# Optimization experiments

Measured on AMD Instinct MI355X. Metric: run time of the kernel, lower is better.

Reference implementation:

```python
import jax, jax.numpy as jnp
import numpy as np
from functools import partial

WARMUP = 365   # init kwarg warmup_length
HYDRODT = 1.0  # daily step

# (name, lower, upper) -- stands in for MODEL_PARAM_DICT['sac']['param_range']
PARAM_RANGES = [
    ("KC", 0.1, 1.2), ("PCTIM", 0.0, 0.1), ("ADIMP", 0.0, 0.3),
    ("UZTWM", 10.0, 100.0), ("UZFWM", 10.0, 100.0), ("LZTWM", 50.0, 400.0),
    ("LZFSM", 10.0, 100.0), ("LZFPM", 50.0, 1000.0), ("RSERV", 0.0, 0.3),
    ("PFREE", 0.0, 0.5), ("RIVA", 0.0, 0.1), ("ZPERC", 5.0, 350.0),
    ("REXP", 1.0, 4.0), ("UZK", 0.1, 0.5), ("LZSK", 0.01, 0.35),
    ("LZPK", 0.001, 0.05), ("CI", 0.5, 0.9), ("CGS", 0.95, 0.998),
    ("CGP", 0.98, 0.998), ("KE", 0.0, 1.0), ("XE", 0.0, 0.5),
]
_LO = np.array([r[1] for r in PARAM_RANGES], dtype=np.float32)
_HI = np.array([r[2] for r in PARAM_RANGES], dtype=np.float32)


def _scale_params(parameters):
    ps = _LO + parameters * (_HI - _LO)  # (n_basin, 21)
    return {name: ps[:, i] for i, (name, _, _) in enumerate(PARAM_RANGES)}


def _sac_step(prm, carry, pe_t):
    (auztw, alztw, uztw, uzfw, lztw, lzfs, lzfp, qs, qi, qgs, qgp, mq) = carry
    kc, pctim, adimp = prm["KC"], prm["PCTIM"], prm["ADIMP"]
    uztwm, uzfwm, lztwm = prm["UZTWM"], prm["UZFWM"], prm["LZTWM"]
    lzfsm, lzfpm = prm["LZFSM"], prm["LZFPM"]
    pfree, riva = prm["PFREE"], prm["RIVA"]
    zperc, rexp, uzk = prm["ZPERC"], prm["REXP"], prm["UZK"]
    lzsk, lzpk = prm["LZSK"], prm["LZPK"]
    ci, cgs, cgp, ke, xe = prm["CI"], prm["CGS"], prm["CGP"], prm["KE"], prm["XE"]

    p = jnp.maximum(pe_t[:, 0], 0.0)
    e = jnp.maximum(jnp.nan_to_num(pe_t[:, 1], nan=0.0, posinf=0.0, neginf=0.0), 0.0)
    ep = kc * e
    # --- impervious / alterable-impervious area ---
    roimp = pctim * p
    ae2 = pctim * ep
    ae1 = jnp.minimum(auztw, ep * (auztw / uztwm))
    ae3 = jnp.maximum((ep - ae1) * (alztw / (uztwm + lztwm)), 0.0)
    pav = jnp.maximum(p - (uztwm - (auztw - ae1)), 0.0)
    adsur = jnp.maximum(pav * ((alztw - ae3) / lztwm), 0.0)
    ars = jnp.maximum(pav - adsur + (alztw - ae3) - lztwm, 0.0)
    auztw = jnp.maximum(jnp.minimum(uztwm, auztw - ae1 + p), 0.0)
    alztw = jnp.maximum(jnp.minimum(lztwm, pav - adsur + (alztw - ae3)), 0.0)
    # --- permeable-area evaporation ---
    e1 = jnp.minimum(uztw, ep * (uztw / uztwm))
    e2 = jnp.maximum(jnp.minimum(uzfw, ep - e1), 0.0)
    e3 = jnp.maximum((ep - e1 - e2) * (lztw / (uztwm + lztwm)), 0.0)
    lt1 = jnp.maximum(lztw - e3, 0.0)
    e4 = riva * ep
    et = ae2 + ae1 + ae3 + e1 + e2 + e3 + e4
    adsur_adimp = adsur * adimp
    ars_adimp = ars * adimp
    parea = 1.0 - pctim - adimp
    # --- permeable-area runoff ---
    rs = jnp.maximum(p + (uztw + uzfw - e1 - e2) - (uztwm + uzfwm), 0.0) * parea
    ut = jnp.maximum(jnp.minimum(uztwm, uztw - e1 + p), 0.0)
    uf = jnp.maximum(jnp.minimum(uzfwm, p + (uztw + uzfw - e1 - e2) - ut), 0.0)
    ri = uf * uzk
    uf = jnp.maximum(uf - ri, 0.0)
    # --- percolation into the lower zone ---
    pbase = lzfsm * lzsk + lzfpm * lzpk
    defr = jnp.maximum(1.0 - (lzfs + lzfp + lt1) / (lzfsm + lzfpm + lztwm), 0.0)
    perc = pbase * (1.0 + zperc * jnp.power(defr, rexp)) * uf / uzfwm
    rate = jnp.maximum(jnp.minimum(perc, (lzfsm + lzfpm + lztwm) - (lzfs + lzfp + lt1)), 0.0)
    uf = jnp.maximum(uf - rate, 0.0)
    fx = jnp.maximum(jnp.minimum(lzfsm + lzfpm - (lzfs + lzfp),
                                 jnp.maximum(rate - (lztwm - lt1), rate * pfree)), 0.0)
    perct = rate - fx
    coef = (lzfpm / (lzfsm + lzfpm)) * (2.0 * (1.0 - lzfp / lzfpm)
           / ((1.0 - lzfp / lzfpm) + (1.0 - lzfs / lzfsm)))
    coef = jnp.minimum(coef, 1.0)
    percp = jnp.maximum(jnp.minimum(lzfpm - lzfp,
                                    jnp.maximum(fx - (lzfsm - lzfs), coef * fx)), 0.0)
    percs = jnp.maximum(fx - percp, 0.0)
    lt = jnp.minimum(lt1 + perct, lztwm)
    ls = lzfs + percs
    lp = lzfp + percp
    rgs = ls * lzsk
    ls = jnp.maximum(ls - rgs, 0.0)
    rgp = lp * lzpk
    lp = jnp.maximum(lp - rgp, 0.0)
    # --- area-weighted runoff components ---
    ri_p, rgs_p, rgp_p = ri * parea, rgs * parea, rgp * parea
    rs_tot = roimp + adsur_adimp + ars_adimp + rs
    # --- slope routing: linear reservoirs ---
    i1 = qs + qi + qgs + qgp  # previous-step total channel inflow
    qs_n = rs_tot
    qi_n = ci * qi + (1.0 - ci) * ri_p
    qgs_n = cgs * qgs + (1.0 - cgs) * rgs_p
    qgp_n = cgp * qgp + (1.0 - cgp) * rgp_p
    i2 = qs_n + qi_n + qgs_n + qgp_n
    # --- river routing: Muskingum, single reach (rivernumber = 1) ---
    dt = 0.5 * HYDRODT
    denom = ke * (1.0 - xe) + dt
    c1 = (ke * xe + dt) / denom
    c2 = (dt - ke * xe) / denom
    c3 = (ke * (1.0 - xe) - dt) / denom
    o1 = mq[:, 0]
    o2 = c1 * i1 + c2 * i2 + c3 * o1
    mq_n = o2[:, None]
    carry_n = (auztw, alztw, ut, uf, lt, ls, lp, qs_n, qi_n, qgs_n, qgp_n, mq_n)
    return carry_n, (et, o2)


def _sac_run(p_and_e, parameters, step_wrap=lambda f: f):
    prm = _scale_params(parameters)
    n_basin = parameters.shape[0]
    s01 = jnp.full((n_basin,), 0.01, dtype=p_and_e.dtype)
    carry = tuple(s01 for _ in range(11)) + (jnp.full((n_basin, 1), 0.01, dtype=p_and_e.dtype),)
    step = step_wrap(partial(_sac_step, prm))
    if WARMUP > 0:
        carry, _ = jax.lax.scan(step, carry, p_and_e[:WARMUP])
        carry = jax.tree_util.tree_map(jax.lax.stop_gradient, carry)  # torch no_grad warmup
    _, (e_sim, q_sim) = jax.lax.scan(step, carry, p_and_e[WARMUP:])
    return jnp.stack([q_sim, e_sim])  # (2, n_step, n_basin)


def setup_inputs() -> dict:
    key = jax.random.key(0)
    k1, k2, k3 = jax.random.split(key, 3)
    T, B = 1825, 10000
    prcp = jax.random.uniform(k1, (T, B), minval=0.0, maxval=20.0)  # mm/day
    pet = jax.random.uniform(k3, (T, B), minval=0.0, maxval=6.0)    # mm/day
    p_and_e = jnp.stack([prcp, pet], axis=-1).astype(jnp.float32)
    parameters = jax.random.uniform(k2, (B, 21), minval=0.01, maxval=0.99).astype(jnp.float32)
    return {"p_and_e": p_and_e, "parameters": parameters}


def reference(p_and_e, parameters):
    return _sac_run(p_and_e, parameters)
```

## Files before the change

kernel.cpp:

```cpp
#include <hip/hip_runtime.h>
#include <math.h>

#define T_TOTAL 1825
#define WARMUP_T 365
#define T_OUT (T_TOTAL - WARMUP_T)
#define NB 10000

__global__ __launch_bounds__(64, 1)
void sac_kernel(const float* __restrict__ p_and_e,
                const float* __restrict__ params,
                float* __restrict__ out)
{
    const int b = blockIdx.x * blockDim.x + threadIdx.x;
    if (b >= NB) return;

    const float* pr = params + b * 21;
    const float kc    = 0.1f   + pr[0]  * (1.2f - 0.1f);
    const float pctim = 0.0f   + pr[1]  * (0.1f - 0.0f);
    const float adimp = 0.0f   + pr[2]  * (0.3f - 0.0f);
    const float uztwm = 10.0f  + pr[3]  * (100.0f - 10.0f);
    const float uzfwm = 10.0f  + pr[4]  * (100.0f - 10.0f);
    const float lztwm = 50.0f  + pr[5]  * (400.0f - 50.0f);
    const float lzfsm = 10.0f  + pr[6]  * (100.0f - 10.0f);
    const float lzfpm = 50.0f  + pr[7]  * (1000.0f - 50.0f);
    const float pfree = 0.0f   + pr[9]  * (0.5f - 0.0f);
    const float riva  = 0.0f   + pr[10] * (0.1f - 0.0f);
    const float zperc = 5.0f   + pr[11] * (350.0f - 5.0f);
    const float rexp  = 1.0f   + pr[12] * (4.0f - 1.0f);
    const float uzk   = 0.1f   + pr[13] * (0.5f - 0.1f);
    const float lzsk  = 0.01f  + pr[14] * (0.35f - 0.01f);
    const float lzpk  = 0.001f + pr[15] * (0.05f - 0.001f);
    const float ci    = 0.5f   + pr[16] * (0.9f - 0.5f);
    const float cgs   = 0.95f  + pr[17] * (0.998f - 0.95f);
    const float cgp   = 0.98f  + pr[18] * (0.998f - 0.98f);
    const float ke    = 0.0f   + pr[19] * (1.0f - 0.0f);
    const float xe    = 0.0f   + pr[20] * (0.5f - 0.0f);

    const float inv_uztwm = 1.0f / uztwm;
    const float inv_lztwm = 1.0f / lztwm;
    const float inv_uzfwm = 1.0f / uzfwm;
    const float inv_uzlz  = 1.0f / (uztwm + lztwm);
    const float uz_sum    = uztwm + uzfwm;
    const float lzall     = lzfsm + lzfpm + lztwm;
    const float inv_lzall = 1.0f / lzall;
    const float lzfsfp    = lzfsm + lzfpm;
    const float ratio_fp  = lzfpm / lzfsfp;
    const float inv_lzfpm = 1.0f / lzfpm;
    const float inv_lzfsm = 1.0f / lzfsm;
    const float pbase     = lzfsm * lzsk + lzfpm * lzpk;
    const float parea     = 1.0f - pctim - adimp;
    const float one_m_ci  = 1.0f - ci;
    const float one_m_cgs = 1.0f - cgs;
    const float one_m_cgp = 1.0f - cgp;
    const float dt    = 0.5f;
    const float denom = ke * (1.0f - xe) + dt;
    const float c1 = (ke * xe + dt) / denom;
    const float c2 = (dt - ke * xe) / denom;
    const float c3 = (ke * (1.0f - xe) - dt) / denom;

    float auztw = 0.01f, alztw = 0.01f;
    float uztw = 0.01f, uzfw = 0.01f, lztw = 0.01f;
    float lzfs = 0.01f, lzfp = 0.01f;
    float qs = 0.01f, qi = 0.01f, qgs = 0.01f, qgp = 0.01f;
    float o_prev = 0.01f;

    const float2* __restrict__ pe2 = (const float2*)p_and_e;
    float* __restrict__ q_out = out;
    float* __restrict__ e_out = out + (size_t)T_OUT * NB;

    unsigned lidx = (unsigned)b;
    unsigned sidx = (unsigned)b;

    auto step = [&](float2 pe, bool do_store) {
        const float p = fmaxf(pe.x, 0.0f);
        const float e = fmaxf(pe.y, 0.0f);

        const float ep    = kc * e;

        const float ae1   = fminf(auztw, ep * (auztw * inv_uztwm));
        const float ae3   = fmaxf((ep - ae1) * (alztw * inv_uzlz), 0.0f);
        const float pav   = fmaxf(p - (uztwm - (auztw - ae1)), 0.0f);
        const float alz3  = alztw - ae3;
        const float adsur = fmaxf(pav * (alz3 * inv_lztwm), 0.0f);
        const float ars   = fmaxf(pav - adsur + alz3 - lztwm, 0.0f);
        const float auztw_n = fmaxf(fminf(uztwm, auztw - ae1 + p), 0.0f);
        const float alztw_n = fmaxf(fminf(lztwm, pav - adsur + alz3), 0.0f);

        const float gp = 1.0f - lzfp * inv_lzfpm;
        const float gs = 1.0f - lzfs * inv_lzfsm;
        float coef = ratio_fp * (2.0f * gp) * __builtin_amdgcn_rcpf(gp + gs);
        coef = fminf(coef, 1.0f);

        const float e1  = fminf(uztw, ep * (uztw * inv_uztwm));
        const float e2  = fmaxf(fminf(uzfw, ep - e1), 0.0f);
        const float e3  = fmaxf((ep - e1 - e2) * (lztw * inv_uzlz), 0.0f);
        const float lt1 = fmaxf(lztw - e3, 0.0f);

        const float uz_avail = p + (uztw + uzfw - e1 - e2);
        const float rs = fmaxf(uz_avail - uz_sum, 0.0f) * parea;
        const float ut = fmaxf(fminf(uztwm, uztw - e1 + p), 0.0f);
        float uf = fmaxf(fminf(uzfwm, uz_avail - ut), 0.0f);
        const float ri = uf * uzk;
        uf = fmaxf(uf - ri, 0.0f);

        const float lzsum = lzfs + lzfp + lt1;
        const float defr  = fmaxf(1.0f - lzsum * inv_lzall, 0.0f);
        const float dpow  = __builtin_amdgcn_exp2f(rexp * __builtin_amdgcn_logf(defr));
        const float perc  = pbase * (1.0f + zperc * dpow) * uf * inv_uzfwm;
        const float rate  = fmaxf(fminf(perc, lzall - lzsum), 0.0f);
        uf = fmaxf(uf - rate, 0.0f);

        const float fx = fmaxf(fminf(lzfsfp - (lzfs + lzfp),
                                     fmaxf(rate - (lztwm - lt1), rate * pfree)),
                               0.0f);
        const float perct = rate - fx;
        const float percp = fmaxf(fminf(lzfpm - lzfp,
                                        fmaxf(fx - (lzfsm - lzfs), coef * fx)),
                                  0.0f);
        const float percs = fmaxf(fx - percp, 0.0f);

        const float lt = fminf(lt1 + perct, lztwm);
        float ls = lzfs + percs;
        float lp = lzfp + percp;
        const float rgs = ls * lzsk;
        ls = fmaxf(ls - rgs, 0.0f);
        const float rgp = lp * lzpk;
        lp = fmaxf(lp - rgp, 0.0f);

        const float ri_p   = ri * parea;
        const float rgs_p  = rgs * parea;
        const float rgp_p  = rgp * parea;
        const float rs_tot = (pctim * p + adsur * adimp) + (ars * adimp + rs);

        const float i1 = (qs + qi) + (qgs + qgp);
        qs  = rs_tot;
        qi  = ci  * qi  + one_m_ci  * ri_p;
        qgs = cgs * qgs + one_m_cgs * rgs_p;
        qgp = cgp * qgp + one_m_cgp * rgp_p;
        const float i2 = (qs + qi) + (qgs + qgp);
        const float o2 = c1 * i1 + c2 * i2 + c3 * o_prev;
        o_prev = o2;

        if (do_store) {
            const float ae2 = pctim * ep;
            const float e4  = riva * ep;
            const float et  = (ae2 + ae1) + (ae3 + e1) + (e2 + e3) + e4;
            q_out[sidx] = o2;
            e_out[sidx] = et;
            sidx += NB;
        }

        auztw = auztw_n; alztw = alztw_n;
        uztw = ut; uzfw = uf; lztw = lt; lzfs = ls; lzfp = lp;
    };

    float2 f0 = pe2[lidx];
    float2 f1 = pe2[lidx + 1u * NB];
    float2 f2 = pe2[lidx + 2u * NB];
    float2 f3 = pe2[lidx + 3u * NB];
    lidx += 4u * NB;

    for (int g = 0; g < 91; ++g) {
        const float2 n0 = pe2[lidx];
        const float2 n1 = pe2[lidx + 1u * NB];
        const float2 n2 = pe2[lidx + 2u * NB];
        const float2 n3 = pe2[lidx + 3u * NB];
        lidx += 4u * NB;
        step(f0, false); step(f1, false); step(f2, false); step(f3, false);
        f0 = n0; f1 = n1; f2 = n2; f3 = n3;
    }
    {
        const float2 n0 = pe2[lidx];
        lidx += NB;
        step(f0, false);
        f0 = f1; f1 = f2; f2 = f3; f3 = n0;
    }

    for (int g = 0; g < 364; ++g) {
        const float2 n0 = pe2[lidx];
        const float2 n1 = pe2[lidx + 1u * NB];
        const float2 n2 = pe2[lidx + 2u * NB];
        const float2 n3 = pe2[lidx + 3u * NB];
        lidx += 4u * NB;
        step(f0, true); step(f1, true); step(f2, true); step(f3, true);
        f0 = n0; f1 = n1; f2 = n2; f3 = n3;
    }
    step(f0, true); step(f1, true); step(f2, true); step(f3, true);
}

extern "C" void kernel_launch(void* const* d_in, const int* in_sizes, int n_in,
                              void* d_out, int out_size, void* d_ws, size_t ws_size,
                              hipStream_t stream) {
    const float* p_and_e = (const float*)d_in[0];
    const float* params  = (const float*)d_in[1];
    float* out = (float*)d_out;

    const int block = 64;
    const int grid = (NB + block - 1) / block;
    sac_kernel<<<grid, block, 0, stream>>>(p_and_e, params, out);
}
```

Measured before the change: 685.6 us.

## Process two basins per thread to interleave independent recurrence chains

Each thread now simulates two basins (b and b+5000), interleaving their time steps so two independent dependency chains can hide each other's ALU and transcendental latency. The grid is halved to about 79 wavefronts, which leaves most CUs on the GPU idle but doubles instruction-level parallelism per wave. Several redundant clamps (fmaxf on quantities already non-negative) were also dropped. The risks are that fewer waves reduce latency hiding of the global loads, and that register pressure roughly doubles.

Measured after the change: 1.088 ms. +58.7%, slower.

```diff
diff --git a/kernel.cpp b/kernel.cpp
--- a/kernel.cpp
+++ b/kernel.cpp
@@ -5,6 +5,154 @@
 #define WARMUP_T 365
 #define T_OUT (T_TOTAL - WARMUP_T)
 #define NB 10000
+#define HALF 5000
+
+
+struct Prm {
+    float kc, pctim, adimp, uztwm, uzfwm, lztwm, lzfsm, lzfpm, pfree, riva,
+          zperc, rexp, uzk, lzsk, lzpk, ci, cgs, cgp;
+    float inv_uztwm, inv_lztwm, inv_uzfwm, inv_uzlz, uz_sum, lzall, inv_lzall,
+          lzfsfp, ratio_fp, inv_lzfpm, inv_lzfsm, pbase, parea,
+          omci, omcgs, omcgp, c1, c2, c3;
+};
+
+struct St {
+    float auztw, alztw, uztw, uzfw, lztw, lzfs, lzfp, qs, qi, qgs, qgp, o_prev;
+};
+
+__device__ __forceinline__ void load_prm(const float* __restrict__ pr, Prm& P)
+{
+    P.kc    = 0.1f   + pr[0]  * (1.2f - 0.1f);
+    P.pctim = 0.0f   + pr[1]  * (0.1f - 0.0f);
+    P.adimp = 0.0f   + pr[2]  * (0.3f - 0.0f);
+    P.uztwm = 10.0f  + pr[3]  * (100.0f - 10.0f);
+    P.uzfwm = 10.0f  + pr[4]  * (100.0f - 10.0f);
+    P.lztwm = 50.0f  + pr[5]  * (400.0f - 50.0f);
+    P.lzfsm = 10.0f  + pr[6]  * (100.0f - 10.0f);
+    P.lzfpm = 50.0f  + pr[7]  * (1000.0f - 50.0f);
+    P.pfree = 0.0f   + pr[9]  * (0.5f - 0.0f);
+    P.riva  = 0.0f   + pr[10] * (0.1f - 0.0f);
+    P.zperc = 5.0f   + pr[11] * (350.0f - 5.0f);
+    P.rexp  = 1.0f   + pr[12] * (4.0f - 1.0f);
+    P.uzk   = 0.1f   + pr[13] * (0.5f - 0.1f);
+    P.lzsk  = 0.01f  + pr[14] * (0.35f - 0.01f);
+    P.lzpk  = 0.001f + pr[15] * (0.05f - 0.001f);
+    P.ci    = 0.5f   + pr[16] * (0.9f - 0.5f);
+    P.cgs   = 0.95f  + pr[17] * (0.998f - 0.95f);
+    P.cgp   = 0.98f  + pr[18] * (0.998f - 0.98f);
+    const float ke = 0.0f + pr[19] * (1.0f - 0.0f);
+    const float xe = 0.0f + pr[20] * (0.5f - 0.0f);
+
+    P.inv_uztwm = 1.0f / P.uztwm;
+    P.inv_lztwm = 1.0f / P.lztwm;
+    P.inv_uzfwm = 1.0f / P.uzfwm;
+    P.inv_uzlz  = 1.0f / (P.uztwm + P.lztwm);
+    P.uz_sum    = P.uztwm + P.uzfwm;
+    P.lzall     = P.lzfsm + P.lzfpm + P.lztwm;
+    P.inv_lzall = 1.0f / P.lzall;
+    P.lzfsfp    = P.lzfsm + P.lzfpm;
+    P.ratio_fp  = P.lzfpm / P.lzfsfp;
+    P.inv_lzfpm = 1.0f / P.lzfpm;
+    P.inv_lzfsm = 1.0f / P.lzfsm;
+    P.pbase     = P.lzfsm * P.lzsk + P.lzfpm * P.lzpk;
+    P.parea     = 1.0f - P.pctim - P.adimp;
+    P.omci      = 1.0f - P.ci;
+    P.omcgs     = 1.0f - P.cgs;
+    P.omcgp     = 1.0f - P.cgp;
+    const float dt    = 0.5f;
+    const float denom = ke * (1.0f - xe) + dt;
+    P.c1 = (ke * xe + dt) / denom;
+    P.c2 = (dt - ke * xe) / denom;
+    P.c3 = (ke * (1.0f - xe) - dt) / denom;
+}
+
+template<bool STORE>
+__device__ __forceinline__ void sac_step(const Prm& P, St& S, const float2 pe,
+                                         float* __restrict__ qp,
+                                         float* __restrict__ eo)
+{
+    const float p = fmaxf(pe.x, 0.0f);
+    const float e = fmaxf(pe.y, 0.0f);
+    const float ep = P.kc * e;
+
+    const float ae1  = fminf(S.auztw, ep * (S.auztw * P.inv_uztwm));
+    const float ae3  = fmaxf((ep - ae1) * (S.alztw * P.inv_uzlz), 0.0f);
+    const float tp   = (S.auztw - ae1) + p;
+    const float pav  = fmaxf(tp - P.uztwm, 0.0f);
+    const float alz3 = S.alztw - ae3;
+    const float adsur = fmaxf(pav * (alz3 * P.inv_lztwm), 0.0f);
+    const float v_   = (pav - adsur) + alz3;
+    const float ars  = fmaxf(v_ - P.lztwm, 0.0f);
+    const float auztw_n = fmaxf(fminf(P.uztwm, tp), 0.0f);
+    const float alztw_n = fmaxf(fminf(P.lztwm, v_), 0.0f);
+
+    const float gp_ = 1.0f - S.lzfp * P.inv_lzfpm;
+    const float gs_ = 1.0f - S.lzfs * P.inv_lzfsm;
+    float coef = P.ratio_fp * (2.0f * gp_) * __builtin_amdgcn_rcpf(gp_ + gs_);
+    coef = fminf(coef, 1.0f);
+
+    const float e1  = fminf(S.uztw, ep * (S.uztw * P.inv_uztwm));
+    const float e2  = fmaxf(fminf(S.uzfw, ep - e1), 0.0f);
+    const float e3  = fmaxf((ep - e1 - e2) * (S.lztw * P.inv_uzlz), 0.0f);
+    const float lt1 = fmaxf(S.lztw - e3, 0.0f);
+
+    const float u_ = (S.uztw - e1) + p;
+    const float uz_avail = u_ + (S.uzfw - e2);
+    const float rs = fmaxf(uz_avail - P.uz_sum, 0.0f) * P.parea;
+    const float ut = fmaxf(fminf(P.uztwm, u_), 0.0f);
+    float uf = fmaxf(fminf(P.uzfwm, uz_avail - ut), 0.0f);
+    const float ri = uf * P.uzk;
+    uf = uf - ri;
+
+    const float lzsum = S.lzfs + S.lzfp + lt1;
+    const float defr  = fmaxf(1.0f - lzsum * P.inv_lzall, 0.0f);
+    const float dpow  = __builtin_amdgcn_exp2f(P.rexp * __builtin_amdgcn_logf(defr));
+    const float perc  = P.pbase * (1.0f + P.zperc * dpow) * uf * P.inv_uzfwm;
+    const float rate  = fmaxf(fminf(perc, P.lzall - lzsum), 0.0f);
+    uf = fmaxf(uf - rate, 0.0f);
+
+    const float fx = fmaxf(fminf(P.lzfsfp - (S.lzfs + S.lzfp),
+                                 fmaxf(rate - (P.lztwm - lt1), rate * P.pfree)),
+                           0.0f);
+    const float perct = rate - fx;
+    const float percp = fmaxf(fminf(P.lzfpm - S.lzfp,
+                                    fmaxf(fx - (P.lzfsm - S.lzfs), coef * fx)),
+                              0.0f);
+    const float percs = fmaxf(fx - percp, 0.0f);
+
+    const float lt = fminf(lt1 + perct, P.lztwm);
+    float ls = S.lzfs + percs;
+    float lp = S.lzfp + percp;
+    const float rgs = ls * P.lzsk;
+    ls = ls - rgs;
+    const float rgp = lp * P.lzpk;
+    lp = lp - rgp;
+
+    const float i1 = (S.qs + S.qi) + (S.qgs + S.qgp);
+    S.qs  = (P.pctim * p + adsur * P.adimp) + (ars * P.adimp + rs);
+    S.qi  = P.ci  * S.qi  + P.omci  * (ri  * P.parea);
+    S.qgs = P.cgs * S.qgs + P.omcgs * (rgs * P.parea);
+    S.qgp = P.cgp * S.qgp + P.omcgp * (rgp * P.parea);
+    const float i2 = (S.qs + S.qi) + (S.qgs + S.qgp);
+    const float o2 = P.c1 * i1 + P.c2 * i2 + P.c3 * S.o_prev;
+    S.o_prev = o2;
+
+    if (STORE) {
+        const float et = (P.pctim * ep + ae1) + (ae3 + e1) + (e2 + e3)
+                       + P.riva * ep;
+        *qp = o2;
+        *eo = et;
+    }
+
+    S.auztw = auztw_n; S.alztw = alztw_n;
+    S.uztw = ut; S.uzfw = uf; S.lztw = lt; S.lzfs = ls; S.lzfp = lp;
+}
+
+__device__ __forceinline__ void init_state(St& S)
+{
+    S.auztw = S.alztw = S.uztw = S.uzfw = S.lztw = 0.01f;
+    S.lzfs = S.lzfp = S.qs = S.qi = S.qgs = S.qgp = S.o_prev = 0.01f;
+}
 
 __global__ __launch_bounds__(64, 1)
 void sac_kernel(const float* __restrict__ p_and_e,
@@ -12,57 +160,15 @@
                 float* __restrict__ out)
 {
     const int b = blockIdx.x * blockDim.x + threadIdx.x;
-    if (b >= NB) return;
-
-    const float* pr = params + b * 21;
-    const float kc    = 0.1f   + pr[0]  * (1.2f - 0.1f);
-    const float pctim = 0.0f   + pr[1]  * (0.1f - 0.0f);
-    const float adimp = 0.0f   + pr[2]  * (0.3f - 0.0f);
-    const float uztwm = 10.0f  + pr[3]  * (100.0f - 10.0f);
-    const float uzfwm = 10.0f  + pr[4]  * (100.0f - 10.0f);
-    const float lztwm = 50.0f  + pr[5]  * (400.0f - 50.0f);
-    const float lzfsm = 10.0f  + pr[6]  * (100.0f - 10.0f);
-    const float lzfpm = 50.0f  + pr[7]  * (1000.0f - 50.0f);
-    const float pfree = 0.0f   + pr[9]  * (0.5f - 0.0f);
-    const float riva  = 0.0f   + pr[10] * (0.1f - 0.0f);
-    const float zperc = 5.0f   + pr[11] * (350.0f - 5.0f);
-    const float rexp  = 1.0f   + pr[12] * (4.0f - 1.0f);
-    const float uzk   = 0.1f   + pr[13] * (0.5f - 0.1f);
-    const float lzsk  = 0.01f  + pr[14] * (0.35f - 0.01f);
-    const float lzpk  = 0.001f + pr[15] * (0.05f - 0.001f);
-    const float ci    = 0.5f   + pr[16] * (0.9f - 0.5f);
-    const float cgs   = 0.95f  + pr[17] * (0.998f - 0.95f);
-    const float cgp   = 0.98f  + pr[18] * (0.998f - 0.98f);
-    const float ke    = 0.0f   + pr[19] * (1.0f - 0.0f);
-    const float xe    = 0.0f   + pr[20] * (0.5f - 0.0f);
-
-    const float inv_uztwm = 1.0f / uztwm;
-    const float inv_lztwm = 1.0f / lztwm;
-    const float inv_uzfwm = 1.0f / uzfwm;
-    const float inv_uzlz  = 1.0f / (uztwm + lztwm);
-    const float uz_sum    = uztwm + uzfwm;
-    const float lzall     = lzfsm + lzfpm + lztwm;
-    const float inv_lzall = 1.0f / lzall;
-    const float lzfsfp    = lzfsm + lzfpm;
-    const float ratio_fp  = lzfpm / lzfsfp;
-    const float inv_lzfpm = 1.0f / lzfpm;
-    const float inv_lzfsm = 1.0f / lzfsm;
-    const float pbase     = lzfsm * lzsk + lzfpm * lzpk;
-    const float parea     = 1.0f - pctim - adimp;
-    const float one_m_ci  = 1.0f - ci;
-    const float one_m_cgs = 1.0f - cgs;
-    const float one_m_cgp = 1.0f - cgp;
-    const float dt    = 0.5f;
-    const float denom = ke * (1.0f - xe) + dt;
-    const float c1 = (ke * xe + dt) / denom;
-    const float c2 = (dt - ke * xe) / denom;
-    const float c3 = (ke * (1.0f - xe) - dt) / denom;
-
-    float auztw = 0.01f, alztw = 0.01f;
-    float uztw = 0.01f, uzfw = 0.01f, lztw = 0.01f;
-    float lzfs = 0.01f, lzfp = 0.01f;
-    float qs = 0.01f, qi = 0.01f, qgs = 0.01f, qgp = 0.01f;
-    float o_prev = 0.01f;
+    if (b >= HALF) return;
+
+    Prm PA, PB;
+    load_prm(params + (size_t)b * 21, PA);
+    load_prm(params + (size_t)(b + HALF) * 21, PB);
+
+    St A, B;
+    init_state(A);
+    init_state(B);
 
     const float2* __restrict__ pe2 = (const float2*)p_and_e;
     float* __restrict__ q_out = out;
@@ -71,121 +177,71 @@
     unsigned lidx = (unsigned)b;
     unsigned sidx = (unsigned)b;
 
-    auto step = [&](float2 pe, bool do_store) {
-        const float p = fmaxf(pe.x, 0.0f);
-        const float e = fmaxf(pe.y, 0.0f);
-
-        const float ep    = kc * e;
-
-        const float ae1   = fminf(auztw, ep * (auztw * inv_uztwm));
-        const float ae3   = fmaxf((ep - ae1) * (alztw * inv_uzlz), 0.0f);
-        const float pav   = fmaxf(p - (uztwm - (auztw - ae1)), 0.0f);
-        const float alz3  = alztw - ae3;
-        const float adsur = fmaxf(pav * (alz3 * inv_lztwm), 0.0f);
-        const float ars   = fmaxf(pav - adsur + alz3 - lztwm, 0.0f);
-        const float auztw_n = fmaxf(fminf(uztwm, auztw - ae1 + p), 0.0f);
-        const float alztw_n = fmaxf(fminf(lztwm, pav - adsur + alz3), 0.0f);
-
-        const float gp = 1.0f - lzfp * inv_lzfpm;
-        const float gs = 1.0f - lzfs * inv_lzfsm;
-        float coef = ratio_fp * (2.0f * gp) * __builtin_amdgcn_rcpf(gp + gs);
-        coef = fminf(coef, 1.0f);
-
-        const float e1  = fminf(uztw, ep * (uztw * inv_uztwm));
-        const float e2  = fmaxf(fminf(uzfw, ep - e1), 0.0f);
-        const float e3  = fmaxf((ep - e1 - e2) * (lztw * inv_uzlz), 0.0f);
-        const float lt1 = fmaxf(lztw - e3, 0.0f);
-
-        const float uz_avail = p + (uztw + uzfw - e1 - e2);
-        const float rs = fmaxf(uz_avail - uz_sum, 0.0f) * parea;
-        const float ut = fmaxf(fminf(uztwm, uztw - e1 + p), 0.0f);
-        float uf = fmaxf(fminf(uzfwm, uz_avail - ut), 0.0f);
-        const float ri = uf * uzk;
-        uf = fmaxf(uf - ri, 0.0f);
-
-        const float lzsum = lzfs + lzfp + lt1;
-        const float defr  = fmaxf(1.0f - lzsum * inv_lzall, 0.0f);
-        const float dpow  = __builtin_amdgcn_exp2f(rexp * __builtin_amdgcn_logf(defr));
-        const float perc  = pbase * (1.0f + zperc * dpow) * uf * inv_uzfwm;
-        const float rate  = fmaxf(fminf(perc, lzall - lzsum), 0.0f);
-        uf = fmaxf(uf - rate, 0.0f);
-
-        const float fx = fmaxf(fminf(lzfsfp - (lzfs + lzfp),
-                                     fmaxf(rate - (lztwm - lt1), rate * pfree)),
-                               0.0f);
-        const float perct = rate - fx;
-        const float percp = fmaxf(fminf(lzfpm - lzfp,
-                                        fmaxf(fx - (lzfsm - lzfs), coef * fx)),
-                                  0.0f);
-        const float percs = fmaxf(fx - percp, 0.0f);
-
-        const float lt = fminf(lt1 + perct, lztwm);
-        float ls = lzfs + percs;
-        float lp = lzfp + percp;
-        const float rgs = ls * lzsk;
-        ls = fmaxf(ls - rgs, 0.0f);
-        const float rgp = lp * lzpk;
-        lp = fmaxf(lp - rgp, 0.0f);
-
-        const float ri_p   = ri * parea;
-        const float rgs_p  = rgs * parea;
-        const float rgp_p  = rgp * parea;
-        const float rs_tot = (pctim * p + adsur * adimp) + (ars * adimp + rs);
-
-        const float i1 = (qs + qi) + (qgs + qgp);
-        qs  = rs_tot;
-        qi  = ci  * qi  + one_m_ci  * ri_p;
-        qgs = cgs * qgs + one_m_cgs * rgs_p;
-        qgp = cgp * qgp + one_m_cgp * rgp_p;
-        const float i2 = (qs + qi) + (qgs + qgp);
-        const float o2 = c1 * i1 + c2 * i2 + c3 * o_prev;
-        o_prev = o2;
-
-        if (do_store) {
-            const float ae2 = pctim * ep;
-            const float e4  = riva * ep;
-            const float et  = (ae2 + ae1) + (ae3 + e1) + (e2 + e3) + e4;
-            q_out[sidx] = o2;
-            e_out[sidx] = et;
-            sidx += NB;
-        }
-
-        auztw = auztw_n; alztw = alztw_n;
-        uztw = ut; uzfw = uf; lztw = lt; lzfs = ls; lzfp = lp;
-    };
-
-    float2 f0 = pe2[lidx];
-    float2 f1 = pe2[lidx + 1u * NB];
-    float2 f2 = pe2[lidx + 2u * NB];
-    float2 f3 = pe2[lidx + 3u * NB];
+    float2 a0 = pe2[lidx];            float2 b0 = pe2[lidx + HALF];
+    float2 a1 = pe2[lidx + 1u*NB];    float2 b1 = pe2[lidx + 1u*NB + HALF];
+    float2 a2 = pe2[lidx + 2u*NB];    float2 b2 = pe2[lidx + 2u*NB + HALF];
+    float2 a3 = pe2[lidx + 3u*NB];    float2 b3 = pe2[lidx + 3u*NB + HALF];
     lidx += 4u * NB;
 
     for (int g = 0; g < 91; ++g) {
-        const float2 n0 = pe2[lidx];
-        const float2 n1 = pe2[lidx + 1u * NB];
-        const float2 n2 = pe2[lidx + 2u * NB];
-        const float2 n3 = pe2[lidx + 3u * NB];
+        const float2 na0 = pe2[lidx];           const float2 nb0 = pe2[lidx + HALF];
+        const float2 na1 = pe2[lidx + 1u*NB];   const float2 nb1 = pe2[lidx + 1u*NB + HALF];
+        const float2 na2 = pe2[lidx + 2u*NB];   const float2 nb2 = pe2[lidx + 2u*NB + HALF];
+        const float2 na3 = pe2[lidx + 3u*NB];   const float2 nb3 = pe2[lidx + 3u*NB + HALF];
         lidx += 4u * NB;
-        step(f0, false); step(f1, false); step(f2, false); step(f3, false);
-        f0 = n0; f1 = n1; f2 = n2; f3 = n3;
+        sac_step<false>(PA, A, a0, nullptr, nullptr);
+        sac_step<false>(PB, B, b0, nullptr, nullptr);
+        sac_step<false>(PA, A, a1, nullptr, nullptr);
+        sac_step<false>(PB, B, b1, nullptr, nullptr);
+        sac_step<false>(PA, A, a2, nullptr, nullptr);
+        sac_step<false>(PB, B, b2, nullptr, nullptr);
+        sac_step<false>(PA, A, a3, nullptr, nullptr);
+        sac_step<false>(PB, B, b3, nullptr, nullptr);
+        a0 = na0; a1 = na1; a2 = na2; a3 = na3;
+        b0 = nb0; b1 = nb1; b2 = nb2; b3 = nb3;
     }
     {
-        const float2 n0 = pe2[lidx];
+        const float2 na = pe2[lidx];
+        const float2 nb = pe2[lidx + HALF];
         lidx += NB;
-        step(f0, false);
-        f0 = f1; f1 = f2; f2 = f3; f3 = n0;
+        sac_step<false>(PA, A, a0, nullptr, nullptr);
+        sac_step<false>(PB, B, b0, nullptr, nullptr);
+        a0 = a1; a1 = a2; a2 = a3; a3 = na;
+        b0 = b1; b1 = b2; b2 = b3; b3 = nb;
     }
 
     for (int g = 0; g < 364; ++g) {
-        const float2 n0 = pe2[lidx];
-        const float2 n1 = pe2[lidx + 1u * NB];
-        const float2 n2 = pe2[lidx + 2u * NB];
-        const float2 n3 = pe2[lidx + 3u * NB];
+        const float2 na0 = pe2[lidx];           const float2 nb0 = pe2[lidx + HALF];
+        const float2 na1 = pe2[lidx + 1u*NB];   const float2 nb1 = pe2[lidx + 1u*NB + HALF];
+        const float2 na2 = pe2[lidx + 2u*NB];   const float2 nb2 = pe2[lidx + 2u*NB + HALF];
+        const float2 na3 = pe2[lidx + 3u*NB];   const float2 nb3 = pe2[lidx + 3u*NB + HALF];
         lidx += 4u * NB;
-        step(f0, true); step(f1, true); step(f2, true); step(f3, true);
-        f0 = n0; f1 = n1; f2 = n2; f3 = n3;
-    }
-    step(f0, true); step(f1, true); step(f2, true); step(f3, true);
+        sac_step<true>(PA, A, a0, q_out + sidx,        e_out + sidx);
+        sac_step<true>(PB, B, b0, q_out + sidx + HALF, e_out + sidx + HALF);
+        sidx += NB;
+        sac_step<true>(PA, A, a1, q_out + sidx,        e_out + sidx);
+        sac_step<true>(PB, B, b1, q_out + sidx + HALF, e_out + sidx + HALF);
+        sidx += NB;
+        sac_step<true>(PA, A, a2, q_out + sidx,        e_out + sidx);
+        sac_step<true>(PB, B, b2, q_out + sidx + HALF, e_out + sidx + HALF);
+        sidx += NB;
+        sac_step<true>(PA, A, a3, q_out + sidx,        e_out + sidx);
+        sac_step<true>(PB, B, b3, q_out + sidx + HALF, e_out + sidx + HALF);
+        sidx += NB;
+        a0 = na0; a1 = na1; a2 = na2; a3 = na3;
+        b0 = nb0; b1 = nb1; b2 = nb2; b3 = nb3;
+    }
+    sac_step<true>(PA, A, a0, q_out + sidx,        e_out + sidx);
+    sac_step<true>(PB, B, b0, q_out + sidx + HALF, e_out + sidx + HALF);
+    sidx += NB;
+    sac_step<true>(PA, A, a1, q_out + sidx,        e_out + sidx);
+    sac_step<true>(PB, B, b1, q_out + sidx + HALF, e_out + sidx + HALF);
+    sidx += NB;
+    sac_step<true>(PA, A, a2, q_out + sidx,        e_out + sidx);
+    sac_step<true>(PB, B, b2, q_out + sidx + HALF, e_out + sidx + HALF);
+    sidx += NB;
+    sac_step<true>(PA, A, a3, q_out + sidx,        e_out + sidx);
+    sac_step<true>(PB, B, b3, q_out + sidx + HALF, e_out + sidx + HALF);
 }
 
 extern "C" void kernel_launch(void* const* d_in, const int* in_sizes, int n_in,
@@ -196,6 +252,6 @@
     float* out = (float*)d_out;
 
     const int block = 64;
-    const int grid = (NB + block - 1) / block;
+    const int grid = (HALF + block - 1) / block;
     sac_kernel<<<grid, block, 0, stream>>>(p_and_e, params, out);
 }
```
